# Kernel optimization log

Measured on AMD Instinct MI355X. Metric: run time of the kernel, lower is better.

## Reference

```python
import jax, jax.numpy as jnp
import numpy as np

N = 50000
E = 800000
D_IN = 128
D_OUT = 64


def setup_inputs() -> dict:
    key = jax.random.key(0)
    ks = jax.random.split(key, 8)
    x = jax.random.normal(ks[0], (N, D_IN), dtype=jnp.float32)
    edge_index = jax.random.randint(ks[1], (2, E), 0, N, dtype=jnp.int64)
    s = 1.0 / np.sqrt(D_IN)
    # PyG SAGEConv: lin_l (applied to aggregated neighbors, has bias), lin_r (root, no bias)
    w1_l = jax.random.uniform(ks[2], (D_IN, D_IN), jnp.float32, -s, s)
    b1 = jnp.zeros((D_IN,), jnp.float32)
    w1_r = jax.random.uniform(ks[3], (D_IN, D_IN), jnp.float32, -s, s)
    w2_l = jax.random.uniform(ks[4], (D_IN, D_OUT), jnp.float32, -s, s)
    b2 = jnp.zeros((D_OUT,), jnp.float32)
    w2_r = jax.random.uniform(ks[5], (D_IN, D_OUT), jnp.float32, -s, s)
    return {"x": x, "edge_index": edge_index, "w1_l": w1_l, "b1": b1,
            "w1_r": w1_r, "w2_l": w2_l, "b2": b2, "w2_r": w2_r}


def _sage_conv(x, src, dst, w_l, b_l, w_r):
    # mean-aggregate source features at destination nodes
    msg_sum = jax.ops.segment_sum(x[src], dst, num_segments=N)  # [N, d]
    cnt = jax.ops.segment_sum(jnp.ones((src.shape[0],), x.dtype), dst, num_segments=N)
    mean = msg_sum / jnp.maximum(cnt, 1.0)[:, None]
    out = mean @ w_l + b_l + x @ w_r
    # L2 normalize (normalize=True)
    norm = jnp.linalg.norm(out, axis=-1, keepdims=True)
    return out / jnp.maximum(norm, 1e-12)


def reference(x, edge_index, w1_l, b1, w1_r, w2_l, b2, w2_r):
    src, dst = edge_index[0], edge_index[1]
    h = _sage_conv(x, src, dst, w1_l, b1, w1_r)
    h = _sage_conv(h, src, dst, w2_l, b2, w2_r)
    return h
```

## Files before the change

kernel.cpp:

```cpp
#include <hip/hip_runtime.h>
#include <math.h>

#define NN 50000
#define EE 800000
#define NB 196
#define CAP 6144

typedef __attribute__((ext_vector_type(8))) short bf16x8;
typedef __attribute__((ext_vector_type(16))) float f32x16;
typedef __attribute__((ext_vector_type(4))) unsigned short us4;

__device__ inline unsigned short bf16_rne(float f) {
    union { float f; unsigned u; } a; a.f = f;
    unsigned u = a.u;
    u += 0x7fff + ((u >> 16) & 1);
    return (unsigned short)(u >> 16);
}
__device__ inline float bf16_lo(unsigned v) {
    union { unsigned u; float f; } a; a.u = v << 16;
    return a.f;
}
__device__ inline float bf16_hi(unsigned v) {
    union { unsigned u; float f; } a; a.u = v & 0xffff0000u;
    return a.f;
}

__global__ __launch_bounds__(1024) void bin_kernel(
        const int* __restrict__ src, const int* __restrict__ dst,
        int* __restrict__ gcur, int* __restrict__ rec, int E) {
    __shared__ int hist[NB];
    __shared__ int cur[NB];
    const int t = threadIdx.x;
    const int per = (E + gridDim.x - 1) / gridDim.x;
    const int lo = blockIdx.x * per;
    const int hi = min(lo + per, E);

    for (int i = t; i < NB; i += 1024) hist[i] = 0;
    __syncthreads();
    for (int e = lo + t; e < hi; e += 1024)
        atomicAdd(&hist[dst[e] >> 8], 1);
    __syncthreads();
    for (int i = t; i < NB; i += 1024)
        cur[i] = atomicAdd(&gcur[i], hist[i]);
    __syncthreads();
    for (int e = lo + t; e < hi; e += 1024) {
        int d = dst[e], s = src[e];
        int cb = d >> 8;
        int p = atomicAdd(&cur[cb], 1);
        if (p < CAP) rec[(size_t)cb * CAP + p] = ((d & 255) << 16) | s;
    }
}

__global__ __launch_bounds__(256) void bucket_deg_scan1_kernel(
        const int* __restrict__ rec, const int* __restrict__ bcur,
        int* __restrict__ deg, int* __restrict__ bsum, int n) {
    __shared__ int cnt[256];
    const int cb = blockIdx.x, t = threadIdx.x;
    cnt[t] = 0;
    __syncthreads();
    int m = bcur[cb]; if (m > CAP) m = CAP;
    const int* r = rec + (size_t)cb * CAP;
    for (int i = t; i < m; i += 256) atomicAdd(&cnt[r[i] >> 16], 1);
    __syncthreads();
    int node = cb * 256 + t;
    int d = cnt[t];
    if (node < n) deg[node] = d;
    __syncthreads();
    for (int ofs = 128; ofs > 0; ofs >>= 1) {
        if (t < ofs) cnt[t] += cnt[t + ofs];
        __syncthreads();
    }
    if (t == 0) bsum[cb] = cnt[0];
}

__global__ void scan2_kernel(int* __restrict__ bsum, int nb) {
    __shared__ int s[256];
    int t = threadIdx.x;
    s[t] = (t < nb) ? bsum[t] : 0;
    __syncthreads();
    for (int ofs = 1; ofs < 256; ofs <<= 1) {
        int v = s[t];
        int a = (t >= ofs) ? s[t - ofs] : 0;
        __syncthreads();
        s[t] = v + a;
        __syncthreads();
    }
    if (t < nb) bsum[t] = (t == 0) ? 0 : s[t - 1];
}

__global__ void scan3_kernel(const int* __restrict__ deg, const int* __restrict__ bsum,
                             int* __restrict__ rowoff, int n) {
    __shared__ int s[256];
    int t = threadIdx.x;
    int i = blockIdx.x * 256 + t;
    int d = (i < n) ? deg[i] : 0;
    s[t] = d;
    __syncthreads();
    for (int ofs = 1; ofs < 256; ofs <<= 1) {
        int v = s[t];
        int a = (t >= ofs) ? s[t - ofs] : 0;
        __syncthreads();
        s[t] = v + a;
        __syncthreads();
    }
    int excl = s[t] - d + bsum[blockIdx.x];
    if (i < n) rowoff[i] = excl;
    if (i == n - 1) rowoff[n] = excl + d;
}

__global__ __launch_bounds__(256) void place_kernel(
        const int* __restrict__ rec, const int* __restrict__ bcur,
        const int* __restrict__ rowoff, unsigned short* __restrict__ csr, int n) {
    __shared__ int cnt[256];
    __shared__ int cur[256];
    __shared__ unsigned short sorted[CAP];
    const int cb = blockIdx.x, t = threadIdx.x;
    int m = bcur[cb]; if (m > CAP) m = CAP;
    const int* r = rec + (size_t)cb * CAP;

    cnt[t] = 0;
    __syncthreads();
    for (int i = t; i < m; i += 256) atomicAdd(&cnt[r[i] >> 16], 1);
    __syncthreads();
    int orig = cnt[t];
    for (int ofs = 1; ofs < 256; ofs <<= 1) {
        int v = cnt[t];
        int a = (t >= ofs) ? cnt[t - ofs] : 0;
        __syncthreads();
        cnt[t] = v + a;
        __syncthreads();
    }
    cur[t] = cnt[t] - orig;
    __syncthreads();
    for (int i = t; i < m; i += 256) {
        int rr = r[i];
        int pos = atomicAdd(&cur[rr >> 16], 1);
        sorted[pos] = (unsigned short)(rr & 0xffff);
    }
    __syncthreads();
    const int base = rowoff[cb * 256];
    for (int i = t; i < m; i += 256) csr[base + i] = sorted[i];
}

__global__ void prep_w_kernel(const float* __restrict__ wl, const float* __restrict__ wr,
                              unsigned short* __restrict__ wt, int HALF, int K) {
    int idx = blockIdx.x * 256 + threadIdx.x;
    int total = 2 * HALF * K;
    if (idx >= total) return;
    int n = idx / K, k = idx % K;
    float v = (n < HALF) ? wl[(size_t)k * HALF + n] : wr[(size_t)k * HALF + (n - HALF)];
    wt[idx] = bf16_rne(v);
}

template <int CO, bool BF16IN>
__global__ __launch_bounds__(256) void transform_mfma_kernel(
        const void* __restrict__ xin, const unsigned short* __restrict__ wt,
        const float* __restrict__ bias, unsigned short* __restrict__ ybuf,
        float* __restrict__ rbuf, int n) {
    constexpr int HALF = CO / 2;
    constexpr int LDW = 136;
    __shared__ unsigned short Xs[64][LDW];
    __shared__ unsigned short Ws[64][LDW];

    const int t = threadIdx.x;
    const int node0 = blockIdx.x * 64;
    const int gy = blockIdx.y;

    if (BF16IN) {
        const unsigned short* xb = (const unsigned short*)xin;
        for (int e = t; e < 64 * 16; e += 256) {
            int nd = e >> 4, c8 = e & 15;
            int node = node0 + nd;
            int4 v = (node < n) ? ((const int4*)(xb + (size_t)node * 128))[c8]
                                : make_int4(0, 0, 0, 0);
            *(int4*)&Xs[nd][c8 * 8] = v;
        }
    } else {
        const float* xf = (const float*)xin;
        for (int e = t; e < 64 * 32; e += 256) {
            int nd = e >> 5, c4 = e & 31;
            int node = node0 + nd;
            float4 v = (node < n) ? ((const float4*)xf)[(size_t)node * 32 + c4]
                                  : make_float4(0.f, 0.f, 0.f, 0.f);
            us4 p;
            p.x = bf16_rne(v.x); p.y = bf16_rne(v.y); p.z = bf16_rne(v.z); p.w = bf16_rne(v.w);
            *(us4*)&Xs[nd][c4 * 4] = p;
        }
    }
    for (int e = t; e < 64 * 16; e += 256) {
        int nd = e >> 4, c8 = e & 15;
        int4 v = ((const int4*)(wt + ((size_t)(gy * 64 + nd)) * 128))[c8];
        *(int4*)&Ws[nd][c8 * 8] = v;
    }
    __syncthreads();

    const int lane = t & 63, wave = t >> 6;
    const int wm = (wave & 1) * 32, wn = (wave >> 1) * 32;
    const int ml = wm + (lane & 31);
    const int nl = wn + (lane & 31);
    const int koff = (lane >> 5) * 8;

    f32x16 acc;
#pragma unroll
    for (int r = 0; r < 16; r++) acc[r] = 0.f;

#pragma unroll
    for (int kk = 0; kk < 8; kk++) {
        bf16x8 a = *(const bf16x8*)&Xs[ml][kk * 16 + koff];
        bf16x8 b = *(const bf16x8*)&Ws[nl][kk * 16 + koff];
        acc = __builtin_amdgcn_mfma_f32_32x32x16_bf16(a, b, acc, 0, 0, 0);
    }

    const int col = gy * 64 + wn + (lane & 31);
    if (col < HALF) {
#pragma unroll
        for (int r = 0; r < 16; r++) {
            int row = (r & 3) + 8 * (r >> 2) + 4 * (lane >> 5);
            int node = node0 + wm + row;
            if (node < n) ybuf[(size_t)node * HALF + col] = bf16_rne(acc[r]);
        }
    } else {
        const float bj = bias[col - HALF];
#pragma unroll
        for (int r = 0; r < 16; r++) {
            int row = (r & 3) + 8 * (r >> 2) + 4 * (lane >> 5);
            int node = node0 + wm + row;
            if (node < n) rbuf[(size_t)node * HALF + (col - HALF)] = acc[r] + bj;
        }
    }
}

template <bool OUTBF16>
__global__ __launch_bounds__(256) void gather128_kernel(
        const unsigned short* __restrict__ y, const float* __restrict__ rr,
        const int* __restrict__ rowoff, const unsigned short* __restrict__ csr,
        void* __restrict__ out, int n) {
    const int wave = threadIdx.x >> 6;
    const int lane = threadIdx.x & 63;
    const int node = blockIdx.x * 4 + wave;
    if (node >= n) return;

    const int off = rowoff[node];
    const int end = rowoff[node + 1];
    const int deg = end - off;

    float2 acc = make_float2(0.f, 0.f);
    for (int k0 = 0; k0 < deg; k0 += 16) {
        int idx[16];
#pragma unroll
        for (int i = 0; i < 16; i++) {
            int kk = off + k0 + i;
            idx[i] = (kk < end) ? (int)csr[kk] : n;
        }
        unsigned v[16];
#pragma unroll
        for (int i = 0; i < 16; i++)
            v[i] = *(const unsigned*)(y + (size_t)idx[i] * 128 + 2 * lane);
#pragma unroll
        for (int i = 0; i < 16; i++) {
            acc.x += bf16_lo(v[i]);
            acc.y += bf16_hi(v[i]);
        }
    }
    float im = 1.0f / fmaxf((float)deg, 1.0f);
    float2 rv = *(const float2*)(rr + (size_t)node * 128 + 2 * lane);
    float2 v = make_float2(acc.x * im + rv.x, acc.y * im + rv.y);
    float s = v.x * v.x + v.y * v.y;
#pragma unroll
    for (int m = 32; m >= 1; m >>= 1) s += __shfl_xor(s, m, 64);
    float rn = 1.0f / fmaxf(sqrtf(s), 1e-12f);
    v.x *= rn; v.y *= rn;
    if (OUTBF16) {
        unsigned pk = (unsigned)bf16_rne(v.x) | ((unsigned)bf16_rne(v.y) << 16);
        *(unsigned*)((unsigned short*)out + (size_t)node * 128 + 2 * lane) = pk;
    } else {
        *(float2*)((float*)out + (size_t)node * 128 + 2 * lane) = v;
    }
}

__global__ __launch_bounds__(256) void gather64_kernel(
        const unsigned short* __restrict__ y, const float* __restrict__ rr,
        const int* __restrict__ rowoff, const unsigned short* __restrict__ csr,
        float* __restrict__ out, int n) {
    const int wave = threadIdx.x >> 6;
    const int lane = threadIdx.x & 63;
    const int node = blockIdx.x * 4 + wave;
    if (node >= n) return;
    const int half = lane >> 5;
    const int l32 = lane & 31;

    const int off = rowoff[node];
    const int end = rowoff[node + 1];
    const int deg = end - off;
    const int P = (deg + 1) >> 1;

    float2 acc = make_float2(0.f, 0.f);
    for (int p0 = 0; p0 < P; p0 += 8) {
        int idx[8];
#pragma unroll
        for (int i = 0; i < 8; i++) {
            int kk = off + 2 * (p0 + i) + half;
            idx[i] = (kk < end) ? (int)csr[kk] : n;
        }
        unsigned v[8];
#pragma unroll
        for (int i = 0; i < 8; i++)
            v[i] = *(const unsigned*)(y + (size_t)idx[i] * 64 + 2 * l32);
#pragma unroll
        for (int i = 0; i < 8; i++) {
            acc.x += bf16_lo(v[i]);
            acc.y += bf16_hi(v[i]);
        }
    }
    acc.x += __shfl_xor(acc.x, 32, 64);
    acc.y += __shfl_xor(acc.y, 32, 64);

    float im = 1.0f / fmaxf((float)deg, 1.0f);
    float2 rv = *(const float2*)(rr + (size_t)node * 64 + 2 * l32);
    float2 v = make_float2(acc.x * im + rv.x, acc.y * im + rv.y);
    float s = v.x * v.x + v.y * v.y;
#pragma unroll
    for (int m = 32; m >= 1; m >>= 1) s += __shfl_xor(s, m, 64);
    s *= 0.5f;
    float rn = 1.0f / fmaxf(sqrtf(s), 1e-12f);
    if (half == 0)
        *(float2*)(out + (size_t)node * 64 + 2 * l32) = make_float2(v.x * rn, v.y * rn);
}

extern "C" void kernel_launch(void* const* d_in, const int* in_sizes, int n_in,
                              void* d_out, int out_size, void* d_ws, size_t ws_size,
                              hipStream_t stream) {
    const float* x   = (const float*)d_in[0];
    const int*   ei  = (const int*)d_in[1];
    const float* w1l = (const float*)d_in[2];
    const float* b1  = (const float*)d_in[3];
    const float* w1r = (const float*)d_in[4];
    const float* w2l = (const float*)d_in[5];
    const float* b2  = (const float*)d_in[6];
    const float* w2r = (const float*)d_in[7];
    float* out = (float*)d_out;

    const int* src = ei;
    const int* dst = ei + EE;

    char* ws = (char*)d_ws;
    auto align = [](size_t v) { return (v + 255) & ~(size_t)255; };
    int*   deg    = (int*)ws;                 size_t o = align((size_t)NN * 4);
    int*   rowoff = (int*)(ws + o);           o += align((size_t)(NN + 1) * 4);
    int*   bcur   = (int*)(ws + o);           o += align((size_t)NB * 4);
    int*   bsum   = (int*)(ws + o);           o += align((size_t)NB * 4);
    int*   rec    = (int*)(ws + o);           o += align((size_t)NB * CAP * 4);
    unsigned short* csr = (unsigned short*)(ws + o); o += align((size_t)EE * 2);
    unsigned short* wt1 = (unsigned short*)(ws + o); o += align((size_t)256 * 128 * 2);
    unsigned short* wt2 = (unsigned short*)(ws + o); o += align((size_t)128 * 128 * 2);
    unsigned short* y1  = (unsigned short*)(ws + o); o += align((size_t)(NN + 1) * 128 * 2);
    float*          r1  = (float*)(ws + o);          o += align((size_t)NN * 128 * 4);
    unsigned short* h1  = (unsigned short*)(ws + o); o += align((size_t)NN * 128 * 2);
    unsigned short* y2  = (unsigned short*)(ws + o); o += align((size_t)(NN + 1) * 64 * 2);
    float*          r2  = (float*)(ws + o);          o += align((size_t)NN * 64 * 4);

    hipMemsetAsync(bcur, 0, (size_t)NB * 4, stream);
    hipMemsetAsync(y1 + (size_t)NN * 128, 0, 256, stream);
    hipMemsetAsync(y2 + (size_t)NN * 64, 0, 128, stream);
    bin_kernel<<<128, 1024, 0, stream>>>(src, dst, bcur, rec, EE);
    bucket_deg_scan1_kernel<<<NB, 256, 0, stream>>>(rec, bcur, deg, bsum, NN);
    scan2_kernel<<<1, 256, 0, stream>>>(bsum, NB);
    scan3_kernel<<<NB, 256, 0, stream>>>(deg, bsum, rowoff, NN);
    place_kernel<<<NB, 256, 0, stream>>>(rec, bcur, rowoff, csr, NN);

    prep_w_kernel<<<(256 * 128 + 255) / 256, 256, 0, stream>>>(w1l, w1r, wt1, 128, 128);
    prep_w_kernel<<<(128 * 128 + 255) / 256, 256, 0, stream>>>(w2l, w2r, wt2, 64, 128);

    transform_mfma_kernel<256, false><<<dim3((NN + 63) / 64, 4), 256, 0, stream>>>(
        x, wt1, b1, y1, r1, NN);
    gather128_kernel<true><<<(NN + 3) / 4, 256, 0, stream>>>(y1, r1, rowoff, csr, h1, NN);

    transform_mfma_kernel<128, true><<<dim3((NN + 63) / 64, 2), 256, 0, stream>>>(
        h1, wt2, b2, y2, r2, NN);
    gather64_kernel<<<(NN + 3) / 4, 256, 0, stream>>>(y2, r2, rowoff, csr, out, NN);
}
```

Measured before the change: 220.5 us.

## Fuse CSR build scans into place kernel and merge prep/memset launches

```diff
diff --git a/kernel.cpp b/kernel.cpp
--- a/kernel.cpp
+++ b/kernel.cpp
@@ -23,6 +23,29 @@
 __device__ inline float bf16_hi(unsigned v) {
     union { unsigned u; float f; } a; a.u = v & 0xffff0000u;
     return a.f;
+}
+
+__global__ void prep_all_kernel(const float* __restrict__ w1l, const float* __restrict__ w1r,
+                                const float* __restrict__ w2l, const float* __restrict__ w2r,
+                                unsigned short* __restrict__ wt1, unsigned short* __restrict__ wt2,
+                                unsigned short* __restrict__ y1pad, unsigned short* __restrict__ y2pad,
+                                int* __restrict__ bcur) {
+    int idx = blockIdx.x * 256 + threadIdx.x;
+    if (idx < 32768) {
+        int n = idx >> 7, k = idx & 127;
+        float v = (n < 128) ? w1l[(size_t)k * 128 + n] : w1r[(size_t)k * 128 + (n - 128)];
+        wt1[idx] = bf16_rne(v);
+    } else if (idx < 49152) {
+        int j = idx - 32768;
+        int n = j >> 7, k = j & 127;
+        float v = (n < 64) ? w2l[(size_t)k * 64 + n] : w2r[(size_t)k * 64 + (n - 64)];
+        wt2[j] = bf16_rne(v);
+    } else {
+        int j = idx - 49152;
+        if (j < 128) y1pad[j] = 0;
+        else if (j < 192) y2pad[j - 128] = 0;
+        else if (j < 192 + NB) bcur[j - 192] = 0;
+    }
 }
 
 __global__ __launch_bounds__(1024) void bin_kernel(
@@ -51,32 +74,10 @@
     }
 }
 
-__global__ __launch_bounds__(256) void bucket_deg_scan1_kernel(
-        const int* __restrict__ rec, const int* __restrict__ bcur,
-        int* __restrict__ deg, int* __restrict__ bsum, int n) {
-    __shared__ int cnt[256];
-    const int cb = blockIdx.x, t = threadIdx.x;
-    cnt[t] = 0;
-    __syncthreads();
-    int m = bcur[cb]; if (m > CAP) m = CAP;
-    const int* r = rec + (size_t)cb * CAP;
-    for (int i = t; i < m; i += 256) atomicAdd(&cnt[r[i] >> 16], 1);
-    __syncthreads();
-    int node = cb * 256 + t;
-    int d = cnt[t];
-    if (node < n) deg[node] = d;
-    __syncthreads();
-    for (int ofs = 128; ofs > 0; ofs >>= 1) {
-        if (t < ofs) cnt[t] += cnt[t + ofs];
-        __syncthreads();
-    }
-    if (t == 0) bsum[cb] = cnt[0];
-}
-
-__global__ void scan2_kernel(int* __restrict__ bsum, int nb) {
+__global__ void scan2_kernel(const int* __restrict__ bcur, int* __restrict__ bsum, int nb) {
     __shared__ int s[256];
     int t = threadIdx.x;
-    s[t] = (t < nb) ? bsum[t] : 0;
+    s[t] = (t < nb) ? bcur[t] : 0;
     __syncthreads();
     for (int ofs = 1; ofs < 256; ofs <<= 1) {
         int v = s[t];
@@ -88,35 +89,17 @@
     if (t < nb) bsum[t] = (t == 0) ? 0 : s[t - 1];
 }
 
-__global__ void scan3_kernel(const int* __restrict__ deg, const int* __restrict__ bsum,
-                             int* __restrict__ rowoff, int n) {
-    __shared__ int s[256];
-    int t = threadIdx.x;
-    int i = blockIdx.x * 256 + t;
-    int d = (i < n) ? deg[i] : 0;
-    s[t] = d;
-    __syncthreads();
-    for (int ofs = 1; ofs < 256; ofs <<= 1) {
-        int v = s[t];
-        int a = (t >= ofs) ? s[t - ofs] : 0;
-        __syncthreads();
-        s[t] = v + a;
-        __syncthreads();
-    }
-    int excl = s[t] - d + bsum[blockIdx.x];
-    if (i < n) rowoff[i] = excl;
-    if (i == n - 1) rowoff[n] = excl + d;
-}
-
 __global__ __launch_bounds__(256) void place_kernel(
         const int* __restrict__ rec, const int* __restrict__ bcur,
-        const int* __restrict__ rowoff, unsigned short* __restrict__ csr, int n) {
+        const int* __restrict__ bsum, int* __restrict__ rowoff,
+        unsigned short* __restrict__ csr, int n) {
     __shared__ int cnt[256];
     __shared__ int cur[256];
     __shared__ unsigned short sorted[CAP];
     const int cb = blockIdx.x, t = threadIdx.x;
     int m = bcur[cb]; if (m > CAP) m = CAP;
     const int* r = rec + (size_t)cb * CAP;
+    const int base = bsum[cb];
 
     cnt[t] = 0;
     __syncthreads();
@@ -130,7 +113,11 @@
         cnt[t] = v + a;
         __syncthreads();
     }
-    cur[t] = cnt[t] - orig;
+    int excl = cnt[t] - orig;
+    int node = cb * 256 + t;
+    if (node < n) rowoff[node] = base + excl;
+    if (node == n - 1) rowoff[n] = base + cnt[t];
+    cur[t] = excl;
     __syncthreads();
     for (int i = t; i < m; i += 256) {
         int rr = r[i];
@@ -138,18 +125,7 @@
         sorted[pos] = (unsigned short)(rr & 0xffff);
     }
     __syncthreads();
-    const int base = rowoff[cb * 256];
     for (int i = t; i < m; i += 256) csr[base + i] = sorted[i];
-}
-
-__global__ void prep_w_kernel(const float* __restrict__ wl, const float* __restrict__ wr,
-                              unsigned short* __restrict__ wt, int HALF, int K) {
-    int idx = blockIdx.x * 256 + threadIdx.x;
-    int total = 2 * HALF * K;
-    if (idx >= total) return;
-    int n = idx / K, k = idx % K;
-    float v = (n < HALF) ? wl[(size_t)k * HALF + n] : wr[(size_t)k * HALF + (n - HALF)];
-    wt[idx] = bf16_rne(v);
 }
 
 template <int CO, bool BF16IN>
@@ -345,8 +321,7 @@
 
     char* ws = (char*)d_ws;
     auto align = [](size_t v) { return (v + 255) & ~(size_t)255; };
-    int*   deg    = (int*)ws;                 size_t o = align((size_t)NN * 4);
-    int*   rowoff = (int*)(ws + o);           o += align((size_t)(NN + 1) * 4);
+    int*   rowoff = (int*)ws;                 size_t o = align((size_t)(NN + 1) * 4);
     int*   bcur   = (int*)(ws + o);           o += align((size_t)NB * 4);
     int*   bsum   = (int*)(ws + o);           o += align((size_t)NB * 4);
     int*   rec    = (int*)(ws + o);           o += align((size_t)NB * CAP * 4);
@@ -359,17 +334,11 @@
     unsigned short* y2  = (unsigned short*)(ws + o); o += align((size_t)(NN + 1) * 64 * 2);
     float*          r2  = (float*)(ws + o);          o += align((size_t)NN * 64 * 4);
 
-    hipMemsetAsync(bcur, 0, (size_t)NB * 4, stream);
-    hipMemsetAsync(y1 + (size_t)NN * 128, 0, 256, stream);
-    hipMemsetAsync(y2 + (size_t)NN * 64, 0, 128, stream);
+    prep_all_kernel<<<194, 256, 0, stream>>>(w1l, w1r, w2l, w2r, wt1, wt2,
+                                             y1 + (size_t)NN * 128, y2 + (size_t)NN * 64, bcur);
     bin_kernel<<<128, 1024, 0, stream>>>(src, dst, bcur, rec, EE);
-    bucket_deg_scan1_kernel<<<NB, 256, 0, stream>>>(rec, bcur, deg, bsum, NN);
-    scan2_kernel<<<1, 256, 0, stream>>>(bsum, NB);
-    scan3_kernel<<<NB, 256, 0, stream>>>(deg, bsum, rowoff, NN);
-    place_kernel<<<NB, 256, 0, stream>>>(rec, bcur, rowoff, csr, NN);
-
-    prep_w_kernel<<<(256 * 128 + 255) / 256, 256, 0, stream>>>(w1l, w1r, wt1, 128, 128);
-    prep_w_kernel<<<(128 * 128 + 255) / 256, 256, 0, stream>>>(w2l, w2r, wt2, 64, 128);
+    scan2_kernel<<<1, 256, 0, stream>>>(bcur, bsum, NB);
+    place_kernel<<<NB, 256, 0, stream>>>(rec, bcur, bsum, rowoff, csr, NN);
 
     transform_mfma_kernel<256, false><<<dim3((NN + 63) / 64, 4), 256, 0, stream>>>(
         x, wt1, b1, y1, r1, NN);
```

Result: faster. 205.5 us (-6.8%).
